# Optimization experiments

Measured on AMD Instinct MI355X. Metric: run time of the kernel, lower is better.

## Reference

```python
import jax, jax.numpy as jnp
import numpy as np

B, N, DIN, HID = 64, 1024, 128, 128
NEG = 9000000000000000.0


def setup_inputs() -> dict:
    key = jax.random.key(0)
    ks = jax.random.split(key, 8)
    s = 1.0 / np.sqrt(DIN)
    x = jax.random.normal(ks[0], (B, N, DIN), dtype=jnp.float32)
    mask = jax.random.randint(ks[1], (B, N, N), 0, 2, dtype=jnp.int32)
    Wv = jax.random.uniform(ks[2], (HID, DIN), jnp.float32, -s, s)
    bv = jax.random.uniform(ks[3], (HID,), jnp.float32, -s, s)
    Wk = jax.random.uniform(ks[4], (HID, DIN), jnp.float32, -s, s)
    bk = jax.random.uniform(ks[5], (HID,), jnp.float32, -s, s)
    Wq = jax.random.uniform(ks[6], (HID, DIN), jnp.float32, -s, s)
    bq = jax.random.uniform(ks[7], (HID,), jnp.float32, -s, s)
    return {"x": x, "mask": mask, "Wv": Wv, "bv": bv, "Wk": Wk, "bk": bk, "Wq": Wq, "bq": bq}


def reference(x, mask, Wv, bv, Wk, bk, Wq, bq):
    m = mask.astype(x.dtype)                       # [B,N,N]
    v = jnp.tanh(jnp.einsum('bnd,hd->bnh', x, Wv) + bv)  # [B,N,H]
    q = jnp.tanh(jnp.einsum('bnd,hd->bnh', x, Wq) + bq)
    k = jnp.tanh(jnp.einsum('bnd,hd->bnh', x, Wk) + bk)
    scores = jnp.einsum('bih,bjh->bij', q, k)      # bmm(q, k^T)
    att = jax.nn.softmax(scores * m - NEG * (1.0 - m), axis=2)
    out = jnp.einsum('bij,bjh->bih', att, v)       # [B,N,H]
    return out
```

## Files before the change

### kernel.cpp

```cpp
#include <hip/hip_runtime.h>
#include <cstdint>
#include <cstddef>

#define BB 64
#define NN 1024
#define DD 128

typedef short    bf16x8 __attribute__((ext_vector_type(8)));
typedef _Float16 f16x8  __attribute__((ext_vector_type(8)));
typedef float    f32x4  __attribute__((ext_vector_type(4)));

__device__ __forceinline__ unsigned short f2bf(float f) {
  union { float f; unsigned u; } v; v.f = f;
  unsigned r = v.u + 0x7FFFu + ((v.u >> 16) & 1u);
  return (unsigned short)(r >> 16);
}
__device__ __forceinline__ unsigned short f2h(float f) {
  union { _Float16 h; unsigned short u; } v; v.h = (_Float16)f;
  return v.u;
}
__device__ __forceinline__ float fast_tanh(float x) {
  x = fminf(15.0f, fmaxf(-15.0f, x));
  float e = __expf(2.0f * x);
  return (e - 1.0f) / (e + 1.0f);
}

__global__ __launch_bounds__(256, 2) void proj_kernel(
    const float* __restrict__ x,
    const float* __restrict__ Wq, const float* __restrict__ bq,
    const float* __restrict__ Wk, const float* __restrict__ bk,
    const float* __restrict__ Wv, const float* __restrict__ bv,
    unsigned short* __restrict__ qg,
    unsigned short* __restrict__ kg,
    unsigned short* __restrict__ vtg)
{
  __shared__ unsigned short wlds[128 * 136];

  const int tid  = threadIdx.x;
  const int lane = tid & 63;
  const int wave = tid >> 6;
  const int quad = lane >> 4;
  const int mr   = lane & 15;
  const int m0   = blockIdx.x * 128;
  const int batch = m0 >> 10;
  const int n0    = m0 & 1023;

  bf16x8 xa[2][4];
#pragma unroll
  for (int mt = 0; mt < 2; ++mt) {
    const float* xr = x + (size_t)(m0 + wave * 32 + mt * 16 + mr) * DD + quad * 8;
#pragma unroll
    for (int ks = 0; ks < 4; ++ks) {
      const float4* xp = (const float4*)(xr + ks * 32);
      float4 f0 = xp[0], f1 = xp[1];
      bf16x8 f;
      f[0] = (short)f2bf(f0.x); f[1] = (short)f2bf(f0.y);
      f[2] = (short)f2bf(f0.z); f[3] = (short)f2bf(f0.w);
      f[4] = (short)f2bf(f1.x); f[5] = (short)f2bf(f1.y);
      f[6] = (short)f2bf(f1.z); f[7] = (short)f2bf(f1.w);
      xa[mt][ks] = f;
    }
  }

  const float* Wp[3] = {Wq, Wk, Wv};
  const float* bp[3] = {bq, bk, bv};

  for (int w = 0; w < 3; ++w) {
    __syncthreads();
    {
      const int row = tid >> 1, half = tid & 1;
      const float* src = Wp[w] + row * 128 + half * 64;
      unsigned short* dst = wlds + row * 136 + half * 64;
#pragma unroll
      for (int c = 0; c < 64; c += 8) {
        const float4* sp = (const float4*)(src + c);
        float4 f0 = sp[0], f1 = sp[1];
        unsigned short tmp[8];
        tmp[0] = f2bf(f0.x); tmp[1] = f2bf(f0.y); tmp[2] = f2bf(f0.z); tmp[3] = f2bf(f0.w);
        tmp[4] = f2bf(f1.x); tmp[5] = f2bf(f1.y); tmp[6] = f2bf(f1.z); tmp[7] = f2bf(f1.w);
        uint4 pk; __builtin_memcpy(&pk, tmp, 16);
        *(uint4*)(dst + c) = pk;
      }
    }
    __syncthreads();

    f32x4 z = {0.f, 0.f, 0.f, 0.f};
    f32x4 acc[2][8];
#pragma unroll
    for (int mt = 0; mt < 2; ++mt)
#pragma unroll
      for (int nt = 0; nt < 8; ++nt) acc[mt][nt] = z;

#pragma unroll
    for (int ks = 0; ks < 4; ++ks) {
#pragma unroll
      for (int nt = 0; nt < 8; ++nt) {
        bf16x8 bfr = *(const bf16x8*)(wlds + (nt * 16 + mr) * 136 + ks * 32 + quad * 8);
        acc[0][nt] = __builtin_amdgcn_mfma_f32_16x16x32_bf16(xa[0][ks], bfr, acc[0][nt], 0, 0, 0);
        acc[1][nt] = __builtin_amdgcn_mfma_f32_16x16x32_bf16(xa[1][ks], bfr, acc[1][nt], 0, 0, 0);
      }
    }

    if (w < 2) {
      unsigned short* outg = (w == 0) ? qg : kg;
#pragma unroll
      for (int mt = 0; mt < 2; ++mt) {
        const int rowbase = m0 + wave * 32 + mt * 16 + quad * 4;
#pragma unroll
        for (int nt = 0; nt < 8; ++nt) {
          float bb = bp[w][nt * 16 + mr];
#pragma unroll
          for (int r = 0; r < 4; ++r) {
            float t = fast_tanh(acc[mt][nt][r] + bb);
            outg[(size_t)(rowbase + r) * DD + nt * 16 + mr] = f2h(t);
          }
        }
      }
    } else {
      __syncthreads();
#pragma unroll
      for (int mt = 0; mt < 2; ++mt) {
        const int ib = wave * 32 + mt * 16 + quad * 4;
#pragma unroll
        for (int nt = 0; nt < 8; ++nt) {
          float bb = bp[2][nt * 16 + mr];
#pragma unroll
          for (int r = 0; r < 4; ++r) {
            float t = fast_tanh(acc[mt][nt][r] + bb);
            wlds[(nt * 16 + mr) * 136 + ib + r] = f2bf(t);
          }
        }
      }
      __syncthreads();
      const int h = tid >> 1, half = tid & 1;
      const unsigned short* src = wlds + h * 136 + half * 64;
      unsigned short* dst = vtg + (size_t)(batch * 128 + h) * NN + n0 + half * 64;
#pragma unroll
      for (int c = 0; c < 64; c += 8)
        *(uint4*)(dst + c) = *(const uint4*)(src + c);
    }
  }
}

__global__ __launch_bounds__(256, 2) void attn_kernel(
    const unsigned short* __restrict__ qg,
    const unsigned short* __restrict__ kg,
    const unsigned short* __restrict__ vtg,
    const int* __restrict__ mask,
    float* __restrict__ out)
{
  __shared__ unsigned short klds[64 * 136];
  __shared__ unsigned short vtlds[144 * 72];
  __shared__ unsigned short plds[128 * 88];

  const int tid  = threadIdx.x;
  const int lane = tid & 63;
  const int wave = tid >> 6;
  const int quad = lane >> 4;
  const int mr   = lane & 15;

  const int bx    = blockIdx.x;
  const int batch = (bx & 7) * 8 + ((bx >> 3) & 7);
  const int i0    = (bx >> 6) * 128;

  for (int idx = tid; idx < 16 * 72; idx += 256) {
    int rr = idx / 72, cc = idx % 72;
    vtlds[(128 + rr) * 72 + cc] = (rr == 0) ? (unsigned short)0x3F80 : (unsigned short)0;
  }

  f16x8 qa[2][4];
#pragma unroll
  for (int mt = 0; mt < 2; ++mt)
#pragma unroll
    for (int ks = 0; ks < 4; ++ks)
      qa[mt][ks] = *(const f16x8*)(qg +
          ((size_t)batch * NN + i0 + wave * 32 + mt * 16 + mr) * DD + ks * 32 + quad * 8);

  f32x4 z = {0.f, 0.f, 0.f, 0.f};
  f32x4 o[2][9];
#pragma unroll
  for (int mt = 0; mt < 2; ++mt)
#pragma unroll
    for (int nt = 0; nt < 9; ++nt) o[mt][nt] = z;

  const unsigned short* kgb = kg  + (size_t)batch * NN * DD;
  const unsigned short* vtb = vtg + (size_t)batch * DD * NN;
  const int* mbase = mask + ((size_t)batch << 20);

  const int kj = tid >> 2, ksg = (tid & 3) * 32;
  const int vh = tid >> 1, vsg = (tid & 1) * 32;

  uint4 kst[4], vst[4];
  {
    const uint4* s1 = (const uint4*)(kgb + (size_t)kj * DD + ksg);
    const uint4* s2 = (const uint4*)(vtb + (size_t)vh * NN + vsg);
#pragma unroll
    for (int c = 0; c < 4; ++c) { kst[c] = s1[c]; vst[c] = s2[c]; }
  }

  for (int t = 0; t < 16; ++t) {
    const int j0 = t * 64;

    int mv[2][4][4];
#pragma unroll
    for (int mt = 0; mt < 2; ++mt) {
      const int* mrow0 = mbase + (size_t)(i0 + wave * 32 + mt * 16 + quad * 4) * NN + j0 + mr;
#pragma unroll
      for (int r = 0; r < 4; ++r)
#pragma unroll
        for (int nt = 0; nt < 4; ++nt)
          mv[mt][nt][r] = mrow0[r * NN + nt * 16];
    }

    __syncthreads();
    {
      uint4* d1 = (uint4*)(klds + kj * 136 + ksg);
      uint4* d2 = (uint4*)(vtlds + vh * 72 + vsg);
#pragma unroll
      for (int c = 0; c < 4; ++c) d1[c] = kst[c];
#pragma unroll
      for (int c = 0; c < 4; ++c) d2[c] = vst[c];
    }
    __syncthreads();

    {
      const int j0n = ((t + 1) & 15) * 64;
      const uint4* s1 = (const uint4*)(kgb + (size_t)(j0n + kj) * DD + ksg);
      const uint4* s2 = (const uint4*)(vtb + (size_t)vh * NN + j0n + vsg);
#pragma unroll
      for (int c = 0; c < 4; ++c) { kst[c] = s1[c]; vst[c] = s2[c]; }
    }

    f32x4 s[2][4];
#pragma unroll
    for (int mt = 0; mt < 2; ++mt)
#pragma unroll
      for (int nt = 0; nt < 4; ++nt) s[mt][nt] = z;
#pragma unroll
    for (int ks = 0; ks < 4; ++ks) {
#pragma unroll
      for (int nt = 0; nt < 4; ++nt) {
        f16x8 kb = *(const f16x8*)(klds + (nt * 16 + mr) * 136 + ks * 32 + quad * 8);
        s[0][nt] = __builtin_amdgcn_mfma_f32_16x16x32_f16(qa[0][ks], kb, s[0][nt], 0, 0, 0);
        s[1][nt] = __builtin_amdgcn_mfma_f32_16x16x32_f16(qa[1][ks], kb, s[1][nt], 0, 0, 0);
      }
    }

#pragma unroll
    for (int mt = 0; mt < 2; ++mt) {
      const int ib = wave * 32 + mt * 16 + quad * 4;
#pragma unroll
      for (int nt = 0; nt < 4; ++nt) {
#pragma unroll
        for (int r = 0; r < 4; ++r) {
          float e = __expf(s[mt][nt][r]);
          e = (mv[mt][nt][r] != 0) ? e : 0.0f;
          plds[(ib + r) * 88 + nt * 16 + mr] = f2bf(e);
        }
      }
    }
    __syncthreads();

#pragma unroll
    for (int ks = 0; ks < 2; ++ks) {
      bf16x8 pa0 = *(const bf16x8*)(plds + (wave * 32 + mr) * 88 + ks * 32 + quad * 8);
      bf16x8 pa1 = *(const bf16x8*)(plds + (wave * 32 + 16 + mr) * 88 + ks * 32 + quad * 8);
#pragma unroll
      for (int nt = 0; nt < 9; ++nt) {
        bf16x8 vb = *(const bf16x8*)(vtlds + (nt * 16 + mr) * 72 + ks * 32 + quad * 8);
        o[0][nt] = __builtin_amdgcn_mfma_f32_16x16x32_bf16(pa0, vb, o[0][nt], 0, 0, 0);
        o[1][nt] = __builtin_amdgcn_mfma_f32_16x16x32_bf16(pa1, vb, o[1][nt], 0, 0, 0);
      }
    }
  }

  float* ob = out + (size_t)batch * NN * DD;
#pragma unroll
  for (int mt = 0; mt < 2; ++mt) {
    const int rowbase = i0 + wave * 32 + mt * 16 + quad * 4;
#pragma unroll
    for (int r = 0; r < 4; ++r) {
      float rs  = __shfl(o[mt][8][r], lane & 48, 64);
      float inv = 1.0f / rs;
#pragma unroll
      for (int nt = 0; nt < 8; ++nt)
        ob[(size_t)(rowbase + r) * DD + nt * 16 + mr] = o[mt][nt][r] * inv;
    }
  }
}

extern "C" void kernel_launch(void* const* d_in, const int* in_sizes, int n_in,
                              void* d_out, int out_size, void* d_ws, size_t ws_size,
                              hipStream_t stream) {
  (void)in_sizes; (void)n_in; (void)out_size; (void)ws_size;
  const float* x  = (const float*)d_in[0];
  const int* mask = (const int*)d_in[1];
  const float* Wv = (const float*)d_in[2];
  const float* bv = (const float*)d_in[3];
  const float* Wk = (const float*)d_in[4];
  const float* bk = (const float*)d_in[5];
  const float* Wq = (const float*)d_in[6];
  const float* bq = (const float*)d_in[7];
  float* out = (float*)d_out;

  unsigned short* qg  = (unsigned short*)d_ws;
  unsigned short* kg  = qg + (size_t)BB * NN * DD;
  unsigned short* vtg = kg + (size_t)BB * NN * DD;

  proj_kernel<<<512, 256, 0, stream>>>(x, Wq, bq, Wk, bk, Wv, bv, qg, kg, vtg);
  attn_kernel<<<512, 256, 0, stream>>>(qg, kg, vtg, mask, out);
}
```

Baseline: 494.0 us.

## Halve attention row tile, alias LDS buffers, and load mask as row-vectors

Halves the attention block's query tile from 128 to 64 rows (one 16-row MFMA tile per wave), doubles the grid to 1024 blocks, and raises the occupancy hint to 4 blocks per CU. K and P now alias the same dynamic LDS region. The mask is read per row as contiguous int4 vectors, packed into a bitmask, and applied to the P fragment in registers. The row sum is accumulated in scalar code, replacing the extra ones-column MFMA tile. The K/V register prefetch is replaced by a load at the top of each iteration. That removes cross-iteration overlap and adds a barrier, in exchange for better occupancy and coalesced mask reads.

Result: slower. 664.2 us (+34.5%).

```diff
diff --git a/kernel.cpp b/kernel.cpp
--- a/kernel.cpp
+++ b/kernel.cpp
@@ -142,16 +142,17 @@
   }
 }
 
-__global__ __launch_bounds__(256, 2) void attn_kernel(
+__global__ __launch_bounds__(256, 4) void attn_kernel(
     const unsigned short* __restrict__ qg,
     const unsigned short* __restrict__ kg,
     const unsigned short* __restrict__ vtg,
     const int* __restrict__ mask,
     float* __restrict__ out)
 {
-  __shared__ unsigned short klds[64 * 136];
-  __shared__ unsigned short vtlds[144 * 72];
-  __shared__ unsigned short plds[128 * 88];
+  extern __shared__ unsigned short lds[];
+  unsigned short* klds = lds;
+  unsigned short* plds = lds;
+  unsigned short* vlds = lds + 8704;
 
   const int tid  = threadIdx.x;
   const int lane = tid & 63;
@@ -160,132 +161,128 @@
   const int mr   = lane & 15;
 
   const int bx    = blockIdx.x;
-  const int batch = (bx & 7) * 8 + ((bx >> 3) & 7);
-  const int i0    = (bx >> 6) * 128;
-
-  for (int idx = tid; idx < 16 * 72; idx += 256) {
-    int rr = idx / 72, cc = idx % 72;
-    vtlds[(128 + rr) * 72 + cc] = (rr == 0) ? (unsigned short)0x3F80 : (unsigned short)0;
-  }
-
-  f16x8 qa[2][4];
-#pragma unroll
-  for (int mt = 0; mt < 2; ++mt)
-#pragma unroll
-    for (int ks = 0; ks < 4; ++ks)
-      qa[mt][ks] = *(const f16x8*)(qg +
-          ((size_t)batch * NN + i0 + wave * 32 + mt * 16 + mr) * DD + ks * 32 + quad * 8);
-
-  f32x4 z = {0.f, 0.f, 0.f, 0.f};
-  f32x4 o[2][9];
-#pragma unroll
-  for (int mt = 0; mt < 2; ++mt)
-#pragma unroll
-    for (int nt = 0; nt < 9; ++nt) o[mt][nt] = z;
+  const int batch = ((bx >> 7) << 3) | (bx & 7);
+  const int i0    = ((bx >> 3) & 15) * 64;
 
   const unsigned short* kgb = kg  + (size_t)batch * NN * DD;
   const unsigned short* vtb = vtg + (size_t)batch * DD * NN;
-  const int* mbase = mask + ((size_t)batch << 20);
+  const int* mrow = mask + ((size_t)batch << 20) + (size_t)(i0 + wave * 16 + mr) * NN;
+
+  f16x8 qa[4];
+#pragma unroll
+  for (int ks = 0; ks < 4; ++ks)
+    qa[ks] = *(const f16x8*)(qg +
+        ((size_t)batch * NN + i0 + wave * 16 + mr) * DD + ks * 32 + quad * 8);
+
+  f32x4 z = {0.f, 0.f, 0.f, 0.f};
+  f32x4 o[8];
+#pragma unroll
+  for (int nt = 0; nt < 8; ++nt) o[nt] = z;
+  float rowsum = 0.0f;
 
   const int kj = tid >> 2, ksg = (tid & 3) * 32;
   const int vh = tid >> 1, vsg = (tid & 1) * 32;
-
-  uint4 kst[4], vst[4];
-  {
-    const uint4* s1 = (const uint4*)(kgb + (size_t)kj * DD + ksg);
-    const uint4* s2 = (const uint4*)(vtb + (size_t)vh * NN + vsg);
-#pragma unroll
-    for (int c = 0; c < 4; ++c) { kst[c] = s1[c]; vst[c] = s2[c]; }
-  }
+  const unsigned short* ksrc = kgb + ksg;
+  const unsigned short* vsrc = vtb + (size_t)vh * NN + vsg;
+
+  int4 mreg[4];
+  mreg[0] = *(const int4*)(mrow + quad * 8);
+  mreg[1] = *(const int4*)(mrow + quad * 8 + 4);
+  mreg[2] = *(const int4*)(mrow + 32 + quad * 8);
+  mreg[3] = *(const int4*)(mrow + 32 + quad * 8 + 4);
 
   for (int t = 0; t < 16; ++t) {
     const int j0 = t * 64;
 
-    int mv[2][4][4];
-#pragma unroll
-    for (int mt = 0; mt < 2; ++mt) {
-      const int* mrow0 = mbase + (size_t)(i0 + wave * 32 + mt * 16 + quad * 4) * NN + j0 + mr;
-#pragma unroll
-      for (int r = 0; r < 4; ++r)
-#pragma unroll
-        for (int nt = 0; nt < 4; ++nt)
-          mv[mt][nt][r] = mrow0[r * NN + nt * 16];
+    uint4 kreg[4], vreg[4];
+    {
+      const uint4* s1 = (const uint4*)(ksrc + (size_t)(j0 + kj) * DD);
+      const uint4* s2 = (const uint4*)(vsrc + j0);
+#pragma unroll
+      for (int c = 0; c < 4; ++c) { kreg[c] = s1[c]; vreg[c] = s2[c]; }
+    }
+
+    unsigned mb = 0;
+#pragma unroll
+    for (int i = 0; i < 4; ++i) {
+      mb |= (unsigned)(mreg[i].x & 1) << (i * 4 + 0);
+      mb |= (unsigned)(mreg[i].y & 1) << (i * 4 + 1);
+      mb |= (unsigned)(mreg[i].z & 1) << (i * 4 + 2);
+      mb |= (unsigned)(mreg[i].w & 1) << (i * 4 + 3);
+    }
+    {
+      const int j0n = ((t + 1) & 15) * 64;
+      mreg[0] = *(const int4*)(mrow + j0n + quad * 8);
+      mreg[1] = *(const int4*)(mrow + j0n + quad * 8 + 4);
+      mreg[2] = *(const int4*)(mrow + j0n + 32 + quad * 8);
+      mreg[3] = *(const int4*)(mrow + j0n + 32 + quad * 8 + 4);
     }
 
     __syncthreads();
     {
       uint4* d1 = (uint4*)(klds + kj * 136 + ksg);
-      uint4* d2 = (uint4*)(vtlds + vh * 72 + vsg);
-#pragma unroll
-      for (int c = 0; c < 4; ++c) d1[c] = kst[c];
-#pragma unroll
-      for (int c = 0; c < 4; ++c) d2[c] = vst[c];
-    }
-    __syncthreads();
-
-    {
-      const int j0n = ((t + 1) & 15) * 64;
-      const uint4* s1 = (const uint4*)(kgb + (size_t)(j0n + kj) * DD + ksg);
-      const uint4* s2 = (const uint4*)(vtb + (size_t)vh * NN + j0n + vsg);
-#pragma unroll
-      for (int c = 0; c < 4; ++c) { kst[c] = s1[c]; vst[c] = s2[c]; }
-    }
-
-    f32x4 s[2][4];
-#pragma unroll
-    for (int mt = 0; mt < 2; ++mt)
-#pragma unroll
-      for (int nt = 0; nt < 4; ++nt) s[mt][nt] = z;
+      uint4* d2 = (uint4*)(vlds + vh * 72 + vsg);
+#pragma unroll
+      for (int c = 0; c < 4; ++c) d1[c] = kreg[c];
+#pragma unroll
+      for (int c = 0; c < 4; ++c) d2[c] = vreg[c];
+    }
+    __syncthreads();
+
+    f32x4 s[4];
+#pragma unroll
+    for (int nt = 0; nt < 4; ++nt) s[nt] = z;
 #pragma unroll
     for (int ks = 0; ks < 4; ++ks) {
 #pragma unroll
       for (int nt = 0; nt < 4; ++nt) {
         f16x8 kb = *(const f16x8*)(klds + (nt * 16 + mr) * 136 + ks * 32 + quad * 8);
-        s[0][nt] = __builtin_amdgcn_mfma_f32_16x16x32_f16(qa[0][ks], kb, s[0][nt], 0, 0, 0);
-        s[1][nt] = __builtin_amdgcn_mfma_f32_16x16x32_f16(qa[1][ks], kb, s[1][nt], 0, 0, 0);
-      }
-    }
-
-#pragma unroll
-    for (int mt = 0; mt < 2; ++mt) {
-      const int ib = wave * 32 + mt * 16 + quad * 4;
-#pragma unroll
-      for (int nt = 0; nt < 4; ++nt) {
-#pragma unroll
-        for (int r = 0; r < 4; ++r) {
-          float e = __expf(s[mt][nt][r]);
-          e = (mv[mt][nt][r] != 0) ? e : 0.0f;
-          plds[(ib + r) * 88 + nt * 16 + mr] = f2bf(e);
-        }
-      }
-    }
-    __syncthreads();
-
-#pragma unroll
-    for (int ks = 0; ks < 2; ++ks) {
-      bf16x8 pa0 = *(const bf16x8*)(plds + (wave * 32 + mr) * 88 + ks * 32 + quad * 8);
-      bf16x8 pa1 = *(const bf16x8*)(plds + (wave * 32 + 16 + mr) * 88 + ks * 32 + quad * 8);
-#pragma unroll
-      for (int nt = 0; nt < 9; ++nt) {
-        bf16x8 vb = *(const bf16x8*)(vtlds + (nt * 16 + mr) * 72 + ks * 32 + quad * 8);
-        o[0][nt] = __builtin_amdgcn_mfma_f32_16x16x32_bf16(pa0, vb, o[0][nt], 0, 0, 0);
-        o[1][nt] = __builtin_amdgcn_mfma_f32_16x16x32_bf16(pa1, vb, o[1][nt], 0, 0, 0);
+        s[nt] = __builtin_amdgcn_mfma_f32_16x16x32_f16(qa[ks], kb, s[nt], 0, 0, 0);
+      }
+    }
+    __syncthreads();
+
+#pragma unroll
+    for (int nt = 0; nt < 4; ++nt) {
+#pragma unroll
+      for (int r = 0; r < 4; ++r)
+        plds[(wave * 16 + quad * 4 + r) * 72 + nt * 16 + mr] = f2bf(__expf(s[nt][r]));
+    }
+    __syncthreads();
+
+#pragma unroll
+    for (int ks2 = 0; ks2 < 2; ++ks2) {
+      bf16x8 pa = *(const bf16x8*)(plds + (wave * 16 + mr) * 72 + ks2 * 32 + quad * 8);
+      bf16x8 pm;
+#pragma unroll
+      for (int e = 0; e < 8; ++e) {
+        unsigned bit = (mb >> (ks2 * 8 + e)) & 1u;
+        short pv = bit ? pa[e] : (short)0;
+        pm[e] = pv;
+        union { unsigned u; float f; } cv;
+        cv.u = ((unsigned)(unsigned short)pv) << 16;
+        rowsum += cv.f;
+      }
+#pragma unroll
+      for (int nt = 0; nt < 8; ++nt) {
+        bf16x8 vb = *(const bf16x8*)(vlds + (nt * 16 + mr) * 72 + ks2 * 32 + quad * 8);
+        o[nt] = __builtin_amdgcn_mfma_f32_16x16x32_bf16(pm, vb, o[nt], 0, 0, 0);
       }
     }
   }
 
-  float* ob = out + (size_t)batch * NN * DD;
-#pragma unroll
-  for (int mt = 0; mt < 2; ++mt) {
-    const int rowbase = i0 + wave * 32 + mt * 16 + quad * 4;
-#pragma unroll
-    for (int r = 0; r < 4; ++r) {
-      float rs  = __shfl(o[mt][8][r], lane & 48, 64);
-      float inv = 1.0f / rs;
-#pragma unroll
-      for (int nt = 0; nt < 8; ++nt)
-        ob[(size_t)(rowbase + r) * DD + nt * 16 + mr] = o[mt][nt][r] * inv;
-    }
+  rowsum += __shfl_xor(rowsum, 16, 64);
+  rowsum += __shfl_xor(rowsum, 32, 64);
+
+  float* ob = out + ((size_t)batch * NN + i0) * DD;
+#pragma unroll
+  for (int r = 0; r < 4; ++r) {
+    float rs  = __shfl(rowsum, quad * 4 + r, 64);
+    float inv = 1.0f / rs;
+    float* orow = ob + (size_t)(wave * 16 + quad * 4 + r) * DD + mr;
+#pragma unroll
+    for (int nt = 0; nt < 8; ++nt)
+      orow[nt * 16] = o[nt][r] * inv;
   }
 }
 
@@ -308,5 +305,5 @@
   unsigned short* vtg = kg + (size_t)BB * NN * DD;
 
   proj_kernel<<<512, 256, 0, stream>>>(x, Wq, bq, Wk, bk, Wv, bv, qg, kg, vtg);
-  attn_kernel<<<512, 256, 0, stream>>>(qg, kg, vtg, mask, out);
-}
+  attn_kernel<<<1024, 256, 35840, stream>>>(qg, kg, vtg, mask, out);
+}
```
